# Performance work log

Hardware: AMD Instinct MI355X
Metric: run time of the kernel (lower is better)

## Reference

```python
import jax, jax.numpy as jnp
import numpy as np

N_USER = 100000
N_ITEM = 50000
N_NODES = N_USER + N_ITEM
N_EDGES = 2000000
N_LAYERS = 3
EMB = 64
BATCH = 2048


def setup_inputs() -> dict:
    key = jax.random.key(0)
    ks = jax.random.split(key, 7)
    return {
        "user_emb": 0.1 * jax.random.normal(ks[0], (N_USER, EMB), dtype=jnp.float32),
        "item_emb": 0.1 * jax.random.normal(ks[1], (N_ITEM, EMB), dtype=jnp.float32),
        "adj_vals": jax.random.uniform(ks[2], (N_EDGES,), dtype=jnp.float32),
        "adj_rows": jax.random.randint(ks[3], (N_EDGES,), 0, N_NODES, dtype=jnp.int32),
        "adj_cols": jax.random.randint(ks[4], (N_EDGES,), 0, N_NODES, dtype=jnp.int32),
        "users": jax.random.randint(ks[5], (BATCH,), 0, N_USER, dtype=jnp.int32),
        "items": jax.random.randint(ks[6], (BATCH,), 0, N_ITEM, dtype=jnp.int32),
    }


def _computer(user_emb, item_emb, adj_vals, adj_rows, adj_cols):
    # LightGCN propagation: emb_{l+1} = A_hat @ emb_l, output = mean over layers 0..L
    all_emb = jnp.concatenate([user_emb, item_emb], axis=0)  # [N, d]
    emb = all_emb
    acc = all_emb
    for _ in range(N_LAYERS):
        msg = adj_vals[:, None] * emb[adj_cols]              # [E, d]
        emb = jax.ops.segment_sum(msg, adj_rows, num_segments=N_NODES)
        acc = acc + emb
    light_out = acc / jnp.float32(N_LAYERS + 1)              # mean over L+1 embeddings
    return light_out[:N_USER], light_out[N_USER:]


def reference(user_emb, item_emb, adj_vals, adj_rows, adj_cols, users, items):
    all_users, all_items = _computer(user_emb, item_emb, adj_vals, adj_rows, adj_cols)
    u = all_users[users]   # [Bu, d]
    i = all_items[items]   # [Bi, d]
    return jax.nn.sigmoid(u @ i.T)  # [Bu, Bi]
```

## Files before the change

kernel.cpp:

```cpp
#include <hip/hip_runtime.h>
#include <hip/hip_bf16.h>


#define EMB 64
#define BSZ 512
#define NBMAX 512
#define BP 2048
#define CAP 8192

__device__ __forceinline__ float bf2f_lo(unsigned int u) {
    return __int_as_float((int)(u << 16));
}
__device__ __forceinline__ float bf2f_hi(unsigned int u) {
    return __int_as_float((int)(u & 0xFFFF0000u));
}
__device__ __forceinline__ float bf2f(unsigned short u) {
    return __int_as_float(((int)u) << 16);
}
__device__ __forceinline__ unsigned short f2bf(float f) {
    union { float f; unsigned int i; } v;
    v.f = f;
    unsigned int lsb = (v.i >> 16) & 1;
    v.i += 0x7fffu + lsb;
    return (unsigned short)(v.i >> 16);
}
__device__ __forceinline__ unsigned int pack2(float a, float b) {
    return (unsigned int)f2bf(a) | ((unsigned int)f2bf(b) << 16);
}

__device__ __forceinline__ int wave_iscan(int v) {
    int lane = threadIdx.x & 63;
#pragma unroll
    for (int off = 1; off < 64; off <<= 1) {
        int x = __shfl_up(v, off, 64);
        if (lane >= off) v += x;
    }
    return v;
}

__global__ void ALGN_init_p1(const float4* __restrict__ ue, const float4* __restrict__ ie,
                             uint4* __restrict__ emb, int* __restrict__ flags, int nFlags,
                             int nUser8, int n8, int initBlocks,
                             const int* __restrict__ rows, int* __restrict__ blockHist,
                             int nE, int seg, int nBuckets) {
    __shared__ int h[NBMAX];
    if (blockIdx.x < initBlocks) {
        int t = blockIdx.x * blockDim.x + threadIdx.x;
        if (t < nFlags) flags[t] = 0;
        if (t >= n8) return;
        float4 a, b;
        if (t < nUser8) { a = ue[2 * t]; b = ue[2 * t + 1]; }
        else           { a = ie[2 * (t - nUser8)]; b = ie[2 * (t - nUser8) + 1]; }
        uint4 o;
        o.x = pack2(a.x, a.y);
        o.y = pack2(a.z, a.w);
        o.z = pack2(b.x, b.y);
        o.w = pack2(b.z, b.w);
        emb[t] = o;
    } else {
        int blk = blockIdx.x - initBlocks;
        for (int i = threadIdx.x; i < nBuckets; i += blockDim.x) h[i] = 0;
        __syncthreads();
        int beg = blk * seg, end = min(beg + seg, nE);
        for (int e = beg + threadIdx.x; e < end; e += blockDim.x)
            atomicAdd(&h[rows[e] >> 9], 1);
        __syncthreads();
        for (int u = threadIdx.x; u < nBuckets; u += blockDim.x)
            blockHist[u * BP + blk] = h[u];
    }
}

__global__ void ALGN_scanA(int* __restrict__ blockHist, int* __restrict__ bucketTotal) {
    __shared__ int wsum[16];
    int b = blockIdx.x, t = threadIdx.x;
    int wid = t >> 6;
    int v0 = blockHist[b * BP + 2 * t];
    int v1 = blockHist[b * BP + 2 * t + 1];
    int s = v0 + v1;
    int isc = wave_iscan(s);
    if ((t & 63) == 63) wsum[wid] = isc;
    __syncthreads();
    if (t < 64) {
        int x = (t < 16) ? wsum[t] : 0;
        x = wave_iscan(x);
        if (t < 16) wsum[t] = x;
    }
    __syncthreads();
    int incl = isc + ((wid > 0) ? wsum[wid - 1] : 0);
    int excl = incl - s;
    blockHist[b * BP + 2 * t]     = excl;
    blockHist[b * BP + 2 * t + 1] = excl + v0;
    if (t == 1023) bucketTotal[b] = incl;
}

__global__ void ALGN_p2(const int* __restrict__ rows, const int* __restrict__ cols,
                        const float* __restrict__ vals,
                        const int* __restrict__ blockHist,
                        int2* __restrict__ part, int nE, int seg, int nBuckets) {
    __shared__ int cur[NBMAX];
    int blk = ((blockIdx.x & 7) * (BP >> 3)) + (blockIdx.x >> 3);
    for (int u = threadIdx.x; u < nBuckets; u += blockDim.x)
        cur[u] = u * CAP + blockHist[u * BP + blk];
    __syncthreads();
    int beg = blk * seg, end = min(beg + seg, nE);
    for (int e = beg + (threadIdx.x << 2); e < end; e += (blockDim.x << 2)) {
        if (e + 4 <= end) {
            int4   r = *(const int4*)(rows + e);
            int4   c = *(const int4*)(cols + e);
            float4 v = *(const float4*)(vals + e);
            int p0 = atomicAdd(&cur[r.x >> 9], 1);
            int p1 = atomicAdd(&cur[r.y >> 9], 1);
            int p2 = atomicAdd(&cur[r.z >> 9], 1);
            int p3 = atomicAdd(&cur[r.w >> 9], 1);
            part[p0] = make_int2(((r.x & 511) << 18) | c.x, __float_as_int(v.x));
            part[p1] = make_int2(((r.y & 511) << 18) | c.y, __float_as_int(v.y));
            part[p2] = make_int2(((r.z & 511) << 18) | c.z, __float_as_int(v.z));
            part[p3] = make_int2(((r.w & 511) << 18) | c.w, __float_as_int(v.w));
        } else {
            for (int k = e; k < end; ++k) {
                int rr = rows[k];
                int pos = atomicAdd(&cur[rr >> 9], 1);
                part[pos] = make_int2(((rr & 511) << 18) | cols[k], __float_as_int(vals[k]));
            }
        }
    }
}

__global__ void ALGN_bsort(const int2* __restrict__ part, const int* __restrict__ bucketTotal,
                           int2* __restrict__ pairs, int* __restrict__ rowPtr,
                           int* __restrict__ rowEnd, int nNodes) {
    __shared__ int st[BSZ];
    __shared__ int wsum[8];
    int b = blockIdx.x, t = threadIdx.x;
    int base = b * CAP;
    int lim  = base + bucketTotal[b];
    if (t < BSZ) st[t] = 0;
    __syncthreads();
    for (int j = base + t; j < lim; j += blockDim.x)
        atomicAdd(&st[part[j].x >> 18], 1);
    __syncthreads();
    int wid = t >> 6;
    int v = (t < BSZ) ? st[t] : 0;
    int isc = wave_iscan(v);
    if ((t & 63) == 63 && wid < 8) wsum[wid] = isc;
    __syncthreads();
    if (t < 64) {
        int s = (t < 8) ? wsum[t] : 0;
        s = wave_iscan(s);
        if (t < 8) wsum[t] = s;
    }
    __syncthreads();
    int excl = isc - v + ((wid > 0 && wid < 8) ? wsum[wid - 1] : 0);
    __syncthreads();
    if (t < BSZ) st[t] = excl;
    int row = b * BSZ + t;
    if (t < BSZ && row < nNodes) {
        rowPtr[row] = base + excl;
        rowEnd[row] = base + excl + v;
    }
    __syncthreads();
    for (int j = base + t; j < lim; j += blockDim.x) {
        int2 p = part[j];
        int lr = p.x >> 18;
        int pos = base + atomicAdd(&st[lr], 1);
        pairs[pos] = make_int2(p.x & 0x3FFFF, p.y);
    }
}

__device__ __forceinline__ void acc8(float& s0, float& s1, float& s2, float& s3,
                                     float& s4, float& s5, float& s6, float& s7,
                                     float v, uint4 x) {
    s0 += v * bf2f_lo(x.x); s1 += v * bf2f_hi(x.x);
    s2 += v * bf2f_lo(x.y); s3 += v * bf2f_hi(x.y);
    s4 += v * bf2f_lo(x.z); s5 += v * bf2f_hi(x.z);
    s6 += v * bf2f_lo(x.w); s7 += v * bf2f_hi(x.w);
}

__device__ __forceinline__ void spmm_row(const uint4* __restrict__ cur,
                                         uint4* __restrict__ next,
                                         const int* __restrict__ rowPtr,
                                         const int* __restrict__ rowEnd,
                                         const int2* __restrict__ pairs,
                                         int row, int fl) {
    int beg = rowPtr[row];
    int end = rowEnd[row];
    float s0 = 0.f, s1 = 0.f, s2 = 0.f, s3 = 0.f;
    float s4 = 0.f, s5 = 0.f, s6 = 0.f, s7 = 0.f;
    int j = beg;
    for (; j + 4 <= end; j += 4) {
        int2 e0 = pairs[j + 0];
        int2 e1 = pairs[j + 1];
        int2 e2 = pairs[j + 2];
        int2 e3 = pairs[j + 3];
        uint4 x0 = cur[(size_t)e0.x * 8 + fl];
        uint4 x1 = cur[(size_t)e1.x * 8 + fl];
        uint4 x2 = cur[(size_t)e2.x * 8 + fl];
        uint4 x3 = cur[(size_t)e3.x * 8 + fl];
        acc8(s0, s1, s2, s3, s4, s5, s6, s7, __int_as_float(e0.y), x0);
        acc8(s0, s1, s2, s3, s4, s5, s6, s7, __int_as_float(e1.y), x1);
        acc8(s0, s1, s2, s3, s4, s5, s6, s7, __int_as_float(e2.y), x2);
        acc8(s0, s1, s2, s3, s4, s5, s6, s7, __int_as_float(e3.y), x3);
    }
    for (; j < end; ++j) {
        int2 e = pairs[j];
        uint4 x = cur[(size_t)e.x * 8 + fl];
        acc8(s0, s1, s2, s3, s4, s5, s6, s7, __int_as_float(e.y), x);
    }
    uint4 o;
    o.x = pack2(s0, s1);
    o.y = pack2(s2, s3);
    o.z = pack2(s4, s5);
    o.w = pack2(s6, s7);
    next[(size_t)row * 8 + fl] = o;
}

__global__ void ALGN_l1fuse(const uint4* __restrict__ curE, uint4* __restrict__ nextE,
                            const int* __restrict__ rowPtr, const int* __restrict__ rowEnd,
                            const int2* __restrict__ pairs, int nNodes, int spmmBlocks,
                            const int* __restrict__ users, const int* __restrict__ items,
                            int* __restrict__ flag2, int batch, int nUser, int markBlocks,
                            const unsigned short* __restrict__ emb0,
                            float* __restrict__ U, float* __restrict__ I) {
    if (blockIdx.x < spmmBlocks) {
        int tid = blockIdx.x * blockDim.x + threadIdx.x;
        int row = tid >> 3;
        int fl  = tid & 7;
        if (row >= nNodes) return;
        spmm_row(curE, nextE, rowPtr, rowEnd, pairs, row, fl);
    } else if (blockIdx.x < spmmBlocks + markBlocks) {
        int tid = (blockIdx.x - spmmBlocks) * blockDim.x + threadIdx.x;
        int idx = tid >> 4;
        int ln  = tid & 15;
        if (idx >= 2 * batch) return;
        int row = (idx < batch) ? users[idx] : (nUser + items[idx - batch]);
        if (ln == 0) flag2[row] = 1;
        int beg = rowPtr[row], end = rowEnd[row];
        for (int j = beg + ln; j < end; j += 16) flag2[pairs[j].x] = 1;
    } else {
        int t = (blockIdx.x - spmmBlocks - markBlocks) * blockDim.x + threadIdx.x;
        if (t >= batch * EMB) return;
        int b = t >> 6, c = t & 63;
        U[t] = bf2f(emb0[users[b] * EMB + c]) * 0.25f;
        I[t] = bf2f(emb0[(nUser + items[b]) * EMB + c]) * 0.25f;
    }
}

__global__ void ALGN_l2fuse(const uint4* __restrict__ curE, uint4* __restrict__ nextE,
                            const int* __restrict__ rowPtr, const int* __restrict__ rowEnd,
                            const int2* __restrict__ pairs, const int* __restrict__ flag,
                            int nNodes, int spmmBlocks,
                            const unsigned short* __restrict__ embGA,
                            const int* __restrict__ users, const int* __restrict__ items,
                            float* __restrict__ U, float* __restrict__ I,
                            int batch, int nUser) {
    if (blockIdx.x < spmmBlocks) {
        int tid = blockIdx.x * blockDim.x + threadIdx.x;
        int row = tid >> 3;
        int fl  = tid & 7;
        if (row >= nNodes) return;
        if (!flag[row]) return;
        spmm_row(curE, nextE, rowPtr, rowEnd, pairs, row, fl);
    } else {
        int t = (blockIdx.x - spmmBlocks) * blockDim.x + threadIdx.x;
        if (t >= batch * EMB) return;
        int b = t >> 6, c = t & 63;
        U[t] += bf2f(embGA[users[b] * EMB + c]) * 0.25f;
        I[t] += bf2f(embGA[(nUser + items[b]) * EMB + c]) * 0.25f;
    }
}

__global__ void ALGN_l3fuse(const uint4* __restrict__ curE, uint4* __restrict__ nextE,
                            const int* __restrict__ rowPtr, const int* __restrict__ rowEnd,
                            const int2* __restrict__ pairs,
                            const int* __restrict__ users, const int* __restrict__ items,
                            int batch, int nUser, int listBlocks,
                            const unsigned short* __restrict__ embGA,
                            float* __restrict__ U, float* __restrict__ I) {
    if (blockIdx.x < listBlocks) {
        int tid = blockIdx.x * blockDim.x + threadIdx.x;
        int idx = tid >> 3;
        int fl  = tid & 7;
        if (idx >= 2 * batch) return;
        int row = (idx < batch) ? users[idx] : (nUser + items[idx - batch]);
        spmm_row(curE, nextE, rowPtr, rowEnd, pairs, row, fl);
    } else {
        int t = (blockIdx.x - listBlocks) * blockDim.x + threadIdx.x;
        if (t >= batch * EMB) return;
        int b = t >> 6, c = t & 63;
        U[t] += bf2f(embGA[users[b] * EMB + c]) * 0.25f;
        I[t] += bf2f(embGA[(nUser + items[b]) * EMB + c]) * 0.25f;
    }
}

__global__ void ALGN_gemm_sigmoid(const float* __restrict__ U, const float* __restrict__ I,
                                  const unsigned short* __restrict__ embL3,
                                  const int* __restrict__ users, const int* __restrict__ items,
                                  float* __restrict__ out, int B, int nUser) {
    __shared__ float su[32][EMB + 1];
    __shared__ float si[32][EMB + 1];
    int tx = threadIdx.x, ty = threadIdx.y;
    int row0 = blockIdx.y * 32, col0 = blockIdx.x * 32;
    int tid = ty * 16 + tx;
    for (int k = tid; k < 32 * EMB; k += 256) {
        int r = k >> 6, c = k & 63;
        int ur = users[row0 + r];
        int ir = items[col0 + r];
        su[r][c] = U[(row0 + r) * EMB + c] + bf2f(embL3[ur * EMB + c]) * 0.25f;
        si[r][c] = I[(col0 + r) * EMB + c] + bf2f(embL3[(nUser + ir) * EMB + c]) * 0.25f;
    }
    __syncthreads();
    float s00 = 0.f, s01 = 0.f, s10 = 0.f, s11 = 0.f;
#pragma unroll
    for (int k = 0; k < EMB; ++k) {
        float a0 = su[2 * ty][k],     a1 = su[2 * ty + 1][k];
        float b0 = si[2 * tx][k],     b1 = si[2 * tx + 1][k];
        s00 += a0 * b0; s01 += a0 * b1;
        s10 += a1 * b0; s11 += a1 * b1;
    }
    int r0 = row0 + 2 * ty, c0 = col0 + 2 * tx;
    out[(size_t)r0 * B + c0]           = 1.f / (1.f + __expf(-s00));
    out[(size_t)r0 * B + c0 + 1]       = 1.f / (1.f + __expf(-s01));
    out[(size_t)(r0 + 1) * B + c0]     = 1.f / (1.f + __expf(-s10));
    out[(size_t)(r0 + 1) * B + c0 + 1] = 1.f / (1.f + __expf(-s11));
}

extern "C" void kernel_launch(void* const* d_in, const int* in_sizes, int n_in,
                              void* d_out, int out_size, void* d_ws, size_t ws_size,
                              hipStream_t stream) {
    const float* user_emb = (const float*)d_in[0];
    const float* item_emb = (const float*)d_in[1];
    const float* adj_vals = (const float*)d_in[2];
    const int*   adj_rows = (const int*)d_in[3];
    const int*   adj_cols = (const int*)d_in[4];
    const int*   users    = (const int*)d_in[5];
    const int*   items    = (const int*)d_in[6];
    float* out = (float*)d_out;

    const int nUserF = in_sizes[0];
    const int nItemF = in_sizes[1];
    const int nEdges = in_sizes[2];
    const int batch  = in_sizes[5];
    const int nUser  = nUserF / EMB;
    const int totalF = nUserF + nItemF;
    const int nNodes = totalF / EMB;
    const int n8     = totalF / 8;
    const int nBuckets = (nNodes + BSZ - 1) / BSZ;
    const int seg    = (((nEdges + BP - 1) / BP) + 3) & ~3;

    unsigned short* embA = (unsigned short*)d_ws;
    unsigned short* embB = embA + totalF;
    float* Ub = (float*)(embB + totalF);
    float* Ib = Ub + (size_t)batch * EMB;
    int2*  pairs = (int2*)(Ib + (size_t)batch * EMB);
    int2*  part  = pairs + (size_t)nBuckets * CAP;
    int*   rowPtr = (int*)(part + (size_t)nBuckets * CAP);
    int*   rowEnd = rowPtr + nNodes;
    int*   blockHist   = rowEnd + nNodes;
    int*   bucketTotal = blockHist + NBMAX * BP;
    int*   flag2 = bucketTotal + NBMAX;

    const int initBlocks = (n8 + 255) / 256;
    ALGN_init_p1<<<initBlocks + BP, 256, 0, stream>>>(
        (const float4*)user_emb, (const float4*)item_emb, (uint4*)embA,
        flag2, nNodes, nUserF / 8, n8, initBlocks,
        adj_rows, blockHist, nEdges, seg, nBuckets);

    ALGN_scanA<<<nBuckets, 1024, 0, stream>>>(blockHist, bucketTotal);

    ALGN_p2<<<BP, 256, 0, stream>>>(adj_rows, adj_cols, adj_vals,
                                    blockHist, part, nEdges, seg, nBuckets);

    ALGN_bsort<<<nBuckets, 1024, 0, stream>>>(part, bucketTotal, pairs,
                                              rowPtr, rowEnd, nNodes);

    const int spmmBlocks = (nNodes * 8 + 255) / 256;
    const int markBlocks = (2 * batch * 16 + 255) / 256;
    const int gaBlocks   = (batch * EMB + 255) / 256;
    const int listBlocks = (2 * batch * 8 + 255) / 256;

    ALGN_l1fuse<<<spmmBlocks + markBlocks + gaBlocks, 256, 0, stream>>>(
        (const uint4*)embA, (uint4*)embB, rowPtr, rowEnd, pairs, nNodes, spmmBlocks,
        users, items, flag2, batch, nUser, markBlocks,
        embA, Ub, Ib);

    ALGN_l2fuse<<<spmmBlocks + gaBlocks, 256, 0, stream>>>(
        (const uint4*)embB, (uint4*)embA, rowPtr, rowEnd, pairs, flag2,
        nNodes, spmmBlocks, embB, users, items, Ub, Ib, batch, nUser);

    ALGN_l3fuse<<<listBlocks + gaBlocks, 256, 0, stream>>>(
        (const uint4*)embA, (uint4*)embB, rowPtr, rowEnd, pairs,
        users, items, batch, nUser, listBlocks,
        embA, Ub, Ib);

    dim3 gg(batch / 32, batch / 32);
    dim3 gb(16, 16);
    ALGN_gemm_sigmoid<<<gg, gb, 0, stream>>>(Ub, Ib, embB, users, items,
                                             out, batch, nUser);
}
```

Measured before the change: 251.6 us.

## Shrink partition blocks, stage buckets in LDS, compact layer-2 rows, retile GEMM

```diff
diff --git a/kernel.cpp b/kernel.cpp
--- a/kernel.cpp
+++ b/kernel.cpp
@@ -5,8 +5,8 @@
 #define EMB 64
 #define BSZ 512
 #define NBMAX 512
-#define BP 2048
-#define CAP 8192
+#define BP 512
+#define CAP 7680
 
 __device__ __forceinline__ float bf2f_lo(unsigned int u) {
     return __int_as_float((int)(u << 16));
@@ -66,31 +66,31 @@
             atomicAdd(&h[rows[e] >> 9], 1);
         __syncthreads();
         for (int u = threadIdx.x; u < nBuckets; u += blockDim.x)
-            blockHist[u * BP + blk] = h[u];
+            blockHist[blk * NBMAX + u] = h[u];
     }
 }
 
 __global__ void ALGN_scanA(int* __restrict__ blockHist, int* __restrict__ bucketTotal) {
-    __shared__ int wsum[16];
+    __shared__ int wsum[4];
     int b = blockIdx.x, t = threadIdx.x;
     int wid = t >> 6;
-    int v0 = blockHist[b * BP + 2 * t];
-    int v1 = blockHist[b * BP + 2 * t + 1];
+    int v0 = blockHist[(2 * t) * NBMAX + b];
+    int v1 = blockHist[(2 * t + 1) * NBMAX + b];
     int s = v0 + v1;
     int isc = wave_iscan(s);
     if ((t & 63) == 63) wsum[wid] = isc;
     __syncthreads();
     if (t < 64) {
-        int x = (t < 16) ? wsum[t] : 0;
+        int x = (t < 4) ? wsum[t] : 0;
         x = wave_iscan(x);
-        if (t < 16) wsum[t] = x;
+        if (t < 4) wsum[t] = x;
     }
     __syncthreads();
     int incl = isc + ((wid > 0) ? wsum[wid - 1] : 0);
     int excl = incl - s;
-    blockHist[b * BP + 2 * t]     = excl;
-    blockHist[b * BP + 2 * t + 1] = excl + v0;
-    if (t == 1023) bucketTotal[b] = incl;
+    blockHist[(2 * t) * NBMAX + b]     = excl;
+    blockHist[(2 * t + 1) * NBMAX + b] = excl + v0;
+    if (t == 255) bucketTotal[b] = incl;
 }
 
 __global__ void ALGN_p2(const int* __restrict__ rows, const int* __restrict__ cols,
@@ -100,7 +100,7 @@
     __shared__ int cur[NBMAX];
     int blk = ((blockIdx.x & 7) * (BP >> 3)) + (blockIdx.x >> 3);
     for (int u = threadIdx.x; u < nBuckets; u += blockDim.x)
-        cur[u] = u * CAP + blockHist[u * BP + blk];
+        cur[u] = u * CAP + blockHist[blk * NBMAX + u];
     __syncthreads();
     int beg = blk * seg, end = min(beg + seg, nE);
     for (int e = beg + (threadIdx.x << 2); e < end; e += (blockDim.x << 2)) {
@@ -129,15 +129,17 @@
 __global__ void ALGN_bsort(const int2* __restrict__ part, const int* __restrict__ bucketTotal,
                            int2* __restrict__ pairs, int* __restrict__ rowPtr,
                            int* __restrict__ rowEnd, int nNodes) {
+    __shared__ int2 ed[CAP];
     __shared__ int st[BSZ];
     __shared__ int wsum[8];
     int b = blockIdx.x, t = threadIdx.x;
     int base = b * CAP;
-    int lim  = base + bucketTotal[b];
+    int total = bucketTotal[b];
+    for (int j = t; j < total; j += blockDim.x) ed[j] = part[base + j];
     if (t < BSZ) st[t] = 0;
     __syncthreads();
-    for (int j = base + t; j < lim; j += blockDim.x)
-        atomicAdd(&st[part[j].x >> 18], 1);
+    for (int j = t; j < total; j += blockDim.x)
+        atomicAdd(&st[ed[j].x >> 18], 1);
     __syncthreads();
     int wid = t >> 6;
     int v = (t < BSZ) ? st[t] : 0;
@@ -159,8 +161,8 @@
         rowEnd[row] = base + excl + v;
     }
     __syncthreads();
-    for (int j = base + t; j < lim; j += blockDim.x) {
-        int2 p = part[j];
+    for (int j = t; j < total; j += blockDim.x) {
+        int2 p = ed[j];
         int lr = p.x >> 18;
         int pos = base + atomicAdd(&st[lr], 1);
         pairs[pos] = make_int2(p.x & 0x3FFFF, p.y);
@@ -214,11 +216,21 @@
     next[(size_t)row * 8 + fl] = o;
 }
 
+__device__ __forceinline__ void addFlag(int row, int* __restrict__ flag2,
+                                        int* __restrict__ list, int* __restrict__ cnt) {
+    if (atomicExch(&flag2[row], 1) == 0) {
+        int p = atomicAdd(cnt, 1);
+        list[p] = row;
+    }
+}
+
 __global__ void ALGN_l1fuse(const uint4* __restrict__ curE, uint4* __restrict__ nextE,
                             const int* __restrict__ rowPtr, const int* __restrict__ rowEnd,
                             const int2* __restrict__ pairs, int nNodes, int spmmBlocks,
                             const int* __restrict__ users, const int* __restrict__ items,
-                            int* __restrict__ flag2, int batch, int nUser, int markBlocks,
+                            int* __restrict__ flag2, int* __restrict__ list,
+                            int* __restrict__ listCount,
+                            int batch, int nUser, int markBlocks,
                             const unsigned short* __restrict__ emb0,
                             float* __restrict__ U, float* __restrict__ I) {
     if (blockIdx.x < spmmBlocks) {
@@ -233,9 +245,10 @@
         int ln  = tid & 15;
         if (idx >= 2 * batch) return;
         int row = (idx < batch) ? users[idx] : (nUser + items[idx - batch]);
-        if (ln == 0) flag2[row] = 1;
+        if (ln == 0) addFlag(row, flag2, list, listCount);
         int beg = rowPtr[row], end = rowEnd[row];
-        for (int j = beg + ln; j < end; j += 16) flag2[pairs[j].x] = 1;
+        for (int j = beg + ln; j < end; j += 16)
+            addFlag(pairs[j].x, flag2, list, listCount);
     } else {
         int t = (blockIdx.x - spmmBlocks - markBlocks) * blockDim.x + threadIdx.x;
         if (t >= batch * EMB) return;
@@ -247,18 +260,19 @@
 
 __global__ void ALGN_l2fuse(const uint4* __restrict__ curE, uint4* __restrict__ nextE,
                             const int* __restrict__ rowPtr, const int* __restrict__ rowEnd,
-                            const int2* __restrict__ pairs, const int* __restrict__ flag,
-                            int nNodes, int spmmBlocks,
+                            const int2* __restrict__ pairs,
+                            const int* __restrict__ list, const int* __restrict__ listCount,
+                            int spmmBlocks,
                             const unsigned short* __restrict__ embGA,
                             const int* __restrict__ users, const int* __restrict__ items,
                             float* __restrict__ U, float* __restrict__ I,
                             int batch, int nUser) {
     if (blockIdx.x < spmmBlocks) {
         int tid = blockIdx.x * blockDim.x + threadIdx.x;
-        int row = tid >> 3;
+        int li  = tid >> 3;
         int fl  = tid & 7;
-        if (row >= nNodes) return;
-        if (!flag[row]) return;
+        if (li >= *listCount) return;
+        int row = list[li];
         spmm_row(curE, nextE, rowPtr, rowEnd, pairs, row, fl);
     } else {
         int t = (blockIdx.x - spmmBlocks) * blockDim.x + threadIdx.x;
@@ -296,12 +310,12 @@
                                   const unsigned short* __restrict__ embL3,
                                   const int* __restrict__ users, const int* __restrict__ items,
                                   float* __restrict__ out, int B, int nUser) {
-    __shared__ float su[32][EMB + 1];
-    __shared__ float si[32][EMB + 1];
+    __shared__ float su[64][EMB + 1];
+    __shared__ float si[64][EMB + 1];
     int tx = threadIdx.x, ty = threadIdx.y;
-    int row0 = blockIdx.y * 32, col0 = blockIdx.x * 32;
+    int row0 = blockIdx.y * 64, col0 = blockIdx.x * 64;
     int tid = ty * 16 + tx;
-    for (int k = tid; k < 32 * EMB; k += 256) {
+    for (int k = tid; k < 64 * EMB; k += 256) {
         int r = k >> 6, c = k & 63;
         int ur = users[row0 + r];
         int ir = items[col0 + r];
@@ -309,19 +323,28 @@
         si[r][c] = I[(col0 + r) * EMB + c] + bf2f(embL3[(nUser + ir) * EMB + c]) * 0.25f;
     }
     __syncthreads();
-    float s00 = 0.f, s01 = 0.f, s10 = 0.f, s11 = 0.f;
+    float acc[4][4] = {};
 #pragma unroll
     for (int k = 0; k < EMB; ++k) {
-        float a0 = su[2 * ty][k],     a1 = su[2 * ty + 1][k];
-        float b0 = si[2 * tx][k],     b1 = si[2 * tx + 1][k];
-        s00 += a0 * b0; s01 += a0 * b1;
-        s10 += a1 * b0; s11 += a1 * b1;
-    }
-    int r0 = row0 + 2 * ty, c0 = col0 + 2 * tx;
-    out[(size_t)r0 * B + c0]           = 1.f / (1.f + __expf(-s00));
-    out[(size_t)r0 * B + c0 + 1]       = 1.f / (1.f + __expf(-s01));
-    out[(size_t)(r0 + 1) * B + c0]     = 1.f / (1.f + __expf(-s10));
-    out[(size_t)(r0 + 1) * B + c0 + 1] = 1.f / (1.f + __expf(-s11));
+        float a[4], bb[4];
+#pragma unroll
+        for (int i = 0; i < 4; ++i) a[i] = su[ty + 16 * i][k];
+#pragma unroll
+        for (int j = 0; j < 4; ++j) bb[j] = si[tx + 16 * j][k];
+#pragma unroll
+        for (int i = 0; i < 4; ++i)
+#pragma unroll
+            for (int j = 0; j < 4; ++j) acc[i][j] += a[i] * bb[j];
+    }
+#pragma unroll
+    for (int i = 0; i < 4; ++i) {
+        int r = row0 + ty + 16 * i;
+#pragma unroll
+        for (int j = 0; j < 4; ++j) {
+            int c = col0 + tx + 16 * j;
+            out[(size_t)r * B + c] = 1.f / (1.f + __expf(-acc[i][j]));
+        }
+    }
 }
 
 extern "C" void kernel_launch(void* const* d_in, const int* in_sizes, int n_in,
@@ -356,16 +379,18 @@
     int*   rowPtr = (int*)(part + (size_t)nBuckets * CAP);
     int*   rowEnd = rowPtr + nNodes;
     int*   blockHist   = rowEnd + nNodes;
-    int*   bucketTotal = blockHist + NBMAX * BP;
+    int*   bucketTotal = blockHist + BP * NBMAX;
     int*   flag2 = bucketTotal + NBMAX;
+    int*   listCount = flag2 + nNodes;
+    int*   list = listCount + 1;
 
     const int initBlocks = (n8 + 255) / 256;
     ALGN_init_p1<<<initBlocks + BP, 256, 0, stream>>>(
         (const float4*)user_emb, (const float4*)item_emb, (uint4*)embA,
-        flag2, nNodes, nUserF / 8, n8, initBlocks,
+        flag2, nNodes + 1, nUserF / 8, n8, initBlocks,
         adj_rows, blockHist, nEdges, seg, nBuckets);
 
-    ALGN_scanA<<<nBuckets, 1024, 0, stream>>>(blockHist, bucketTotal);
+    ALGN_scanA<<<nBuckets, 256, 0, stream>>>(blockHist, bucketTotal);
 
     ALGN_p2<<<BP, 256, 0, stream>>>(adj_rows, adj_cols, adj_vals,
                                     blockHist, part, nEdges, seg, nBuckets);
@@ -380,19 +405,19 @@
 
     ALGN_l1fuse<<<spmmBlocks + markBlocks + gaBlocks, 256, 0, stream>>>(
         (const uint4*)embA, (uint4*)embB, rowPtr, rowEnd, pairs, nNodes, spmmBlocks,
-        users, items, flag2, batch, nUser, markBlocks,
+        users, items, flag2, list, listCount, batch, nUser, markBlocks,
         embA, Ub, Ib);
 
     ALGN_l2fuse<<<spmmBlocks + gaBlocks, 256, 0, stream>>>(
-        (const uint4*)embB, (uint4*)embA, rowPtr, rowEnd, pairs, flag2,
-        nNodes, spmmBlocks, embB, users, items, Ub, Ib, batch, nUser);
+        (const uint4*)embB, (uint4*)embA, rowPtr, rowEnd, pairs,
+        list, listCount, spmmBlocks, embB, users, items, Ub, Ib, batch, nUser);
 
     ALGN_l3fuse<<<listBlocks + gaBlocks, 256, 0, stream>>>(
         (const uint4*)embA, (uint4*)embB, rowPtr, rowEnd, pairs,
         users, items, batch, nUser, listBlocks,
         embA, Ub, Ib);
 
-    dim3 gg(batch / 32, batch / 32);
+    dim3 gg(batch / 64, batch / 64);
     dim3 gb(16, 16);
     ALGN_gemm_sigmoid<<<gg, gb, 0, stream>>>(Ub, Ib, embB, users, items,
                                              out, batch, nUser);
```

After: 273.8 us. 1.09x slower.
